# Optimization experiments

Hardware: AMD Instinct MI355X
Metric: run time of the kernel (lower is better)

## Reference

```python
import jax, jax.numpy as jnp
import numpy as np

N = 25000   # nodes
E = 100000  # edges
FN = 32     # num_node_features
FE = 16     # num_edge_features
DH = 32     # node_hidden_channels (= edge_hidden_channels)
H = 4       # gat heads
DG = 8      # gat hidden per head (H*DG == DH)
C = 10      # num_classes


def setup_inputs() -> dict:
    key = jax.random.key(0)
    ks = jax.random.split(key, 25)
    f = lambda k, s: (jax.random.normal(k, s, dtype=jnp.float32) * 0.1)
    inp = {
        "x": jax.random.normal(ks[0], (N, FN), dtype=jnp.float32),
        "edge_attr": jax.random.normal(ks[1], (E, FE), dtype=jnp.float32),
        "edge_index": jax.random.randint(ks[2], (2, E), 0, N, dtype=jnp.int32),
        # node / edge encoders
        "We_node": f(ks[3], (FN, DH)), "be_node": f(ks[4], (DH,)),
        "We_edge": f(ks[5], (FE, DH)), "be_edge": f(ks[6], (DH,)),
        # conv1 (NNConv): edge MLP -> [DH*DH], root weight, bias
        "W1_nn": f(ks[7], (DH, DH * DH)), "b1_nn": f(ks[8], (DH * DH,)),
        "root1": f(ks[9], (DH, DH)), "bias1": f(ks[10], (DH,)),
        # GATv2Conv: lin_l, lin_r (with bias), attention vector, output bias
        "Wl": f(ks[11], (DH, H * DG)), "bl": f(ks[12], (H * DG,)),
        "Wr": f(ks[13], (DH, H * DG)), "br": f(ks[14], (H * DG,)),
        "att": f(ks[15], (H, DG)), "bias_gat": f(ks[16], (H * DG,)),
        # conv2 (NNConv): in = H*DG = 32, out = DH = 32
        "W2_nn": f(ks[17], (DH, H * DG * DH)), "b2_nn": f(ks[18], (H * DG * DH,)),
        "root2": f(ks[19], (H * DG, DH)), "bias2": f(ks[20], (DH,)),
        # final classifier
        "Wlin": f(ks[21], (DH, C)), "blin": f(ks[22], (C,)),
    }
    return inp


def _forward(x, edge_attr, edge_index, We_node, be_node, We_edge, be_edge,
             W1_nn, b1_nn, root1, bias1, Wl, bl, Wr, br, att, bias_gat,
             W2_nn, b2_nn, root2, bias2, Wlin, blin):
    src, dst = edge_index[0], edge_index[1]  # message flows src -> dst
    h = x @ We_node + be_node                # [N, DH]
    ea = edge_attr @ We_edge + be_edge       # [E, DH]

    # ---- NNConv 1: per-edge weight matrices + scatter-add, root + bias ----
    W1 = (ea @ W1_nn + b1_nn).reshape(E, DH, DH)       # [E, DH, DH]
    msg = jnp.einsum('ei,eio->eo', h[src], W1)          # [E, DH]
    agg = jax.ops.segment_sum(msg, dst, num_segments=N)
    h = jax.nn.relu(agg + h @ root1 + bias1)

    # ---- GATv2Conv (adds self loops, like PyG default) ----
    loops = jnp.arange(N, dtype=src.dtype)
    si = jnp.concatenate([src, loops])
    di = jnp.concatenate([dst, loops])
    xl = (h @ Wl + bl).reshape(N, H, DG)
    xr = (h @ Wr + br).reshape(N, H, DG)
    e = jax.nn.leaky_relu(xl[si] + xr[di], negative_slope=0.2)  # [E2, H, DG]
    logits = jnp.einsum('ehd,hd->eh', e, att)                   # [E2, H]
    m = jax.lax.stop_gradient(jax.ops.segment_max(logits, di, num_segments=N))
    m = jnp.where(jnp.isfinite(m), m, 0.0)
    a = jnp.exp(logits - m[di])
    denom = jax.ops.segment_sum(a, di, num_segments=N)
    alpha = a / (denom[di] + 1e-16)                             # segment softmax over dst
    out = jax.ops.segment_sum(xl[si] * alpha[:, :, None], di, num_segments=N)
    h = jax.nn.relu(out.reshape(N, H * DG) + bias_gat)

    # ---- NNConv 2 ----
    W2 = (ea @ W2_nn + b2_nn).reshape(E, H * DG, DH)
    msg2 = jnp.einsum('ei,eio->eo', h[src], W2)
    agg2 = jax.ops.segment_sum(msg2, dst, num_segments=N)
    h = jax.nn.relu(agg2 + h @ root2 + bias2)

    return h @ Wlin + blin


def reference(x, edge_attr, edge_index, We_node, be_node, We_edge, be_edge,
              W1_nn, b1_nn, root1, bias1, Wl, bl, Wr, br, att, bias_gat,
              W2_nn, b2_nn, root2, bias2, Wlin, blin):
    return _forward(x, edge_attr, edge_index, We_node, be_node, We_edge, be_edge,
                    W1_nn, b1_nn, root1, bias1, Wl, bl, Wr, br, att, bias_gat,
                    W2_nn, b2_nn, root2, bias2, Wlin, blin)
```

## Files before the change

### kernel.cpp

```cpp
#include <hip/hip_runtime.h>
#include <hip/hip_bf16.h>
#include <math.h>

#define NN 25000
#define NE 100000
#define NTILES (NE / 16)
#define NBN 98
#define NBE 391
#define NBP 264
#define NBC 391

typedef __attribute__((ext_vector_type(8))) short short8;
typedef __attribute__((ext_vector_type(4))) float f32x4;

static __device__ __forceinline__ short8 pack_bf8(const float* p) {
  union { short8 s; unsigned int u[4]; } r;
#pragma unroll
  for (int q = 0; q < 4; q++)
    asm("v_cvt_pk_bf16_f32 %0, %1, %2" : "=v"(r.u[q]) : "v"(p[2 * q]), "v"(p[2 * q + 1]));
  return r.s;
}

__global__ void __launch_bounds__(256) k_zero(int* __restrict__ deg) {
  int n = blockIdx.x * 256 + threadIdx.x;
  if (n < NN) deg[n] = 0;
}

__global__ void __launch_bounds__(256) k_prep(
    const float* __restrict__ x, const float* __restrict__ eattr,
    const int* __restrict__ ei,
    const float* __restrict__ We_node, const float* __restrict__ be_node,
    const float* __restrict__ We_edge, const float* __restrict__ be_edge,
    const float* __restrict__ root1, const float* __restrict__ bias1,
    const float* __restrict__ W1, const float* __restrict__ b1,
    const float* __restrict__ W2, const float* __restrict__ b2,
    float* __restrict__ h0, float* __restrict__ r1pre, float* __restrict__ ea,
    __hip_bfloat16* __restrict__ Bswz1, __hip_bfloat16* __restrict__ Bswz2,
    int* __restrict__ deg) {
  int b = blockIdx.x;
  int tid = threadIdx.x;
  if (b < NBN) {
    int n = b * 256 + tid;
    if (n >= NN) return;
    float xv[32], hv[32], rv[32];
#pragma unroll
    for (int i = 0; i < 8; i++) *(float4*)(xv + 4 * i) = *(const float4*)(x + n * 32 + 4 * i);
#pragma unroll
    for (int j = 0; j < 32; j++) hv[j] = be_node[j];
#pragma unroll
    for (int i = 0; i < 32; i++) {
      float xi = xv[i];
#pragma unroll
      for (int j = 0; j < 32; j++) hv[j] += xi * We_node[i * 32 + j];
    }
#pragma unroll
    for (int i = 0; i < 8; i++) *(float4*)(h0 + n * 32 + 4 * i) = *(float4*)(hv + 4 * i);
#pragma unroll
    for (int j = 0; j < 32; j++) rv[j] = bias1[j];
#pragma unroll
    for (int i = 0; i < 32; i++) {
      float hi = hv[i];
#pragma unroll
      for (int j = 0; j < 32; j++) rv[j] += hi * root1[i * 32 + j];
    }
#pragma unroll
    for (int i = 0; i < 8; i++) *(float4*)(r1pre + n * 32 + 4 * i) = *(float4*)(rv + 4 * i);
  } else if (b < NBN + NBE) {
    int e = (b - NBN) * 256 + tid;
    if (e >= NE) return;
    float av[16], ov[32];
#pragma unroll
    for (int i = 0; i < 4; i++) *(float4*)(av + 4 * i) = *(const float4*)(eattr + e * 16 + 4 * i);
#pragma unroll
    for (int j = 0; j < 32; j++) ov[j] = be_edge[j];
#pragma unroll
    for (int k = 0; k < 16; k++) {
      float ak = av[k];
#pragma unroll
      for (int j = 0; j < 32; j++) ov[j] += ak * We_edge[k * 32 + j];
    }
#pragma unroll
    for (int i = 0; i < 8; i++) *(float4*)(ea + e * 32 + 4 * i) = *(float4*)(ov + 4 * i);
  } else if (b < NBN + NBE + NBP) {
    int idx = (b - NBN - NBE) * 256 + tid;
    if (idx >= 2 * 33792) return;
    int sel = idx >= 33792;
    int r = idx - sel * 33792;
    int j = r & 7;
    int l = (r >> 3) & 63;
    int nt = (r >> 9) & 1;
    int t = r >> 10;
    int i = 8 * (l >> 4) + j;
    int o = nt * 16 + (l & 15);
    const float* W = sel ? W2 : W1;
    const float* bb = sel ? b2 : b1;
    float v = (t < 32) ? W[t * 1024 + i * 32 + o] : bb[i * 32 + o];
    (sel ? Bswz2 : Bswz1)[r] = __float2bfloat16(v);
  } else {
    int e = (b - NBN - NBE - NBP) * 256 + tid;
    if (e < NE) atomicAdd(&deg[ei[NE + e]], 1);
  }
}

__global__ void __launch_bounds__(256) k_scan1(const int* __restrict__ deg,
                                               int* __restrict__ bsum) {
  __shared__ int s[256];
  int tid = threadIdx.x;
  int n = blockIdx.x * 256 + tid;
  s[tid] = (n < NN) ? deg[n] : 0;
  __syncthreads();
  for (int d = 128; d > 0; d >>= 1) {
    if (tid < d) s[tid] += s[tid + d];
    __syncthreads();
  }
  if (tid == 0) bsum[blockIdx.x] = s[0];
}

__global__ void __launch_bounds__(256) k_scan3(const int* __restrict__ deg,
                                               const int* __restrict__ bsum,
                                               int* __restrict__ off,
                                               int* __restrict__ cursor) {
  __shared__ int sb[128];
  __shared__ int s[256];
  int tid = threadIdx.x;
  if (tid < 128) sb[tid] = (tid < NBN) ? bsum[tid] : 0;
  int n = blockIdx.x * 256 + tid;
  int v = (n < NN) ? deg[n] : 0;
  s[tid] = v;
  __syncthreads();
  for (int d = 1; d < 128; d <<= 1) {
    int t = 0;
    if (tid < 128 && tid >= d) t = sb[tid - d];
    __syncthreads();
    if (tid < 128) sb[tid] += t;
    __syncthreads();
  }
  for (int d = 1; d < 256; d <<= 1) {
    int t = (tid >= d) ? s[tid - d] : 0;
    __syncthreads();
    s[tid] += t;
    __syncthreads();
  }
  int base = (blockIdx.x > 0) ? sb[blockIdx.x - 1] : 0;
  int excl = s[tid] - v + base;
  if (n < NN) { off[n] = excl; cursor[n] = excl; }
}

__global__ void k_csr_fill(const int* __restrict__ ei, int* __restrict__ cursor,
                           int* __restrict__ slot, int* __restrict__ perm) {
  int e = blockIdx.x * blockDim.x + threadIdx.x;
  if (e >= NE) return;
  int d = ei[NE + e];
  int p = atomicAdd(&cursor[d], 1);
  slot[p] = e;
  perm[e] = p;
}

__global__ void __launch_bounds__(256) k_nnconv_mfma(
    const float* __restrict__ hin, const float* __restrict__ ea,
    const __hip_bfloat16* __restrict__ Bswz, const int* __restrict__ ei,
    const int* __restrict__ perm, float* __restrict__ msgbuf) {
  extern __shared__ short8 bsh[];
  int tid = threadIdx.x;
  {
    uint4* s4 = (uint4*)bsh;
    const uint4* g4 = (const uint4*)Bswz;
#pragma unroll
    for (int it = 0; it < 16; it++) s4[tid + 256 * it] = g4[tid + 256 * it];
  }
  __syncthreads();

  int wid = tid >> 6;
  int lane = tid & 63;
  int lrow = lane & 15;
  int lk8 = (lane >> 4) * 8;

  for (int tile = blockIdx.x * 4 + wid; tile < NTILES; tile += gridDim.x * 4) {
    int e0 = tile * 16;
    int e = e0 + lrow;
    int src = ei[e];
    float hf[8];
    *(float4*)(hf)     = *(const float4*)(hin + src * 32 + lk8);
    *(float4*)(hf + 4) = *(const float4*)(hin + src * 32 + lk8 + 4);
    float eav[32];
#pragma unroll
    for (int c = 0; c < 8; c++)
      *(float4*)(eav + 4 * c) = *(const float4*)(ea + e * 32 + 4 * c);
    short8 af_bias = pack_bf8(hf);

    f32x4 a00 = {0.f, 0.f, 0.f, 0.f}, a01 = a00, a10 = a00, a11 = a00;
#pragma unroll
    for (int t = 0; t < 32; t++) {
      float et = eav[t];
      float pr[8];
#pragma unroll
      for (int j = 0; j < 8; j++) pr[j] = et * hf[j];
      short8 af = pack_bf8(pr);
      short8 b0 = bsh[(t * 2 + 0) * 64 + lane];
      short8 b1 = bsh[(t * 2 + 1) * 64 + lane];
      if (t & 1) {
        a01 = __builtin_amdgcn_mfma_f32_16x16x32_bf16(af, b0, a01, 0, 0, 0);
        a11 = __builtin_amdgcn_mfma_f32_16x16x32_bf16(af, b1, a11, 0, 0, 0);
      } else {
        a00 = __builtin_amdgcn_mfma_f32_16x16x32_bf16(af, b0, a00, 0, 0, 0);
        a10 = __builtin_amdgcn_mfma_f32_16x16x32_bf16(af, b1, a10, 0, 0, 0);
      }
    }
    {
      const short8* gb = (const short8*)Bswz;
      short8 b0 = gb[(32 * 2 + 0) * 64 + lane];
      short8 b1 = gb[(32 * 2 + 1) * 64 + lane];
      a00 = __builtin_amdgcn_mfma_f32_16x16x32_bf16(af_bias, b0, a00, 0, 0, 0);
      a10 = __builtin_amdgcn_mfma_f32_16x16x32_bf16(af_bias, b1, a10, 0, 0, 0);
    }
    f32x4 c0 = a00 + a01;
    f32x4 c1 = a10 + a11;
    int r0 = (lane >> 4) * 4;
#pragma unroll
    for (int r = 0; r < 4; r++) {
      int p = perm[e0 + r0 + r];
      float* mp = msgbuf + p * 32 + lrow;
      mp[0]  = c0[r];
      mp[16] = c1[r];
    }
  }
}

__global__ void __launch_bounds__(256) k_node1(
    const float* __restrict__ r1pre, const float* __restrict__ msgbuf,
    const int* __restrict__ off, const int* __restrict__ deg,
    const float* __restrict__ Wl, const float* __restrict__ bl,
    const float* __restrict__ Wr, const float* __restrict__ br,
    float* __restrict__ xl, float* __restrict__ xr) {
  int t = blockIdx.x * blockDim.x + threadIdx.x;
  if (t >= 2 * NN) return;
  int n = t >> 1, half = t & 1;
  int c0 = half * 16;
  float hv[16];
  const float* rp = r1pre + n * 32 + c0;
#pragma unroll
  for (int i = 0; i < 4; i++) *(float4*)(hv + 4 * i) = *(const float4*)(rp + 4 * i);
  int o0 = off[n], o1 = o0 + deg[n];
  for (int idx = o0; idx < o1; idx++) {
    const float* mp = msgbuf + idx * 32 + c0;
#pragma unroll
    for (int i = 0; i < 4; i++) {
      float4 mv = *(const float4*)(mp + 4 * i);
      hv[4 * i + 0] += mv.x; hv[4 * i + 1] += mv.y;
      hv[4 * i + 2] += mv.z; hv[4 * i + 3] += mv.w;
    }
  }
#pragma unroll
  for (int j = 0; j < 16; j++) hv[j] = fmaxf(hv[j], 0.f);
  float a0[16], a1[16];
#pragma unroll
  for (int j = 0; j < 16; j++) {
    float o = __shfl_xor(hv[j], 1);
    a0[j] = half ? o : hv[j];
    a1[j] = half ? hv[j] : o;
  }
  const float* W = half ? Wr : Wl;
  const float* bb = half ? br : bl;
  float ov[32];
#pragma unroll
  for (int j = 0; j < 32; j++) ov[j] = bb[j];
#pragma unroll
  for (int i = 0; i < 16; i++) {
    float u = a0[i], v = a1[i];
#pragma unroll
    for (int j = 0; j < 32; j++)
      ov[j] += u * W[i * 32 + j] + v * W[(16 + i) * 32 + j];
  }
  float* dst = (half ? xr : xl) + n * 32;
#pragma unroll
  for (int i = 0; i < 8; i++) *(float4*)(dst + 4 * i) = *(float4*)(ov + 4 * i);
}

__global__ void __launch_bounds__(256) k_gat_node(
    const int* __restrict__ ei, const int* __restrict__ slot,
    const float* __restrict__ xl, const float* __restrict__ xr,
    const int* __restrict__ off, const int* __restrict__ deg,
    const float* __restrict__ att, const float* __restrict__ bias_gat,
    float* __restrict__ h2) {
  int t = blockIdx.x * blockDim.x + threadIdx.x;
  if (t >= 4 * NN) return;
  int n = t >> 2, hh = t & 3;
  const float* xrp = xr + n * 32 + hh * 8;
  const float* xsp = xl + n * 32 + hh * 8;
  const float* atp = att + hh * 8;
  float xrv[8], attv[8], xself[8];
  *(float4*)(xrv)      = *(const float4*)(xrp);
  *(float4*)(xrv + 4)  = *(const float4*)(xrp + 4);
  *(float4*)(attv)     = *(const float4*)(atp);
  *(float4*)(attv + 4) = *(const float4*)(atp + 4);
  *(float4*)(xself)    = *(const float4*)(xsp);
  *(float4*)(xself + 4)= *(const float4*)(xsp + 4);
  float slg = 0.f;
#pragma unroll
  for (int dg = 0; dg < 8; dg++) {
    float v = xself[dg] + xrv[dg];
    v = (v > 0.f) ? v : 0.2f * v;
    slg += v * attv[dg];
  }
  float w0 = __expf(slg);
  float den = w0;
  float accv[8];
#pragma unroll
  for (int dg = 0; dg < 8; dg++) accv[dg] = w0 * xself[dg];
  int o0 = off[n], o1 = o0 + deg[n];
  for (int idx = o0; idx < o1; idx++) {
    int s = ei[slot[idx]];
    const float* xp = xl + s * 32 + hh * 8;
    float xv[8];
    *(float4*)(xv)     = *(const float4*)(xp);
    *(float4*)(xv + 4) = *(const float4*)(xp + 4);
    float lg = 0.f;
#pragma unroll
    for (int dg = 0; dg < 8; dg++) {
      float v = xv[dg] + xrv[dg];
      v = (v > 0.f) ? v : 0.2f * v;
      lg += v * attv[dg];
    }
    float w = __expf(lg);
    den += w;
#pragma unroll
    for (int dg = 0; dg < 8; dg++) accv[dg] += w * xv[dg];
  }
  float sc = 1.f / (den + 1e-16f);
  float hv[8];
#pragma unroll
  for (int dg = 0; dg < 8; dg++)
    hv[dg] = fmaxf(accv[dg] * sc + bias_gat[hh * 8 + dg], 0.f);
  float* op = h2 + n * 32 + hh * 8;
  *(float4*)(op)     = *(float4*)(hv);
  *(float4*)(op + 4) = *(float4*)(hv + 4);
}

__global__ void __launch_bounds__(256) k_node2(
    const float* __restrict__ h2, const float* __restrict__ msgbuf,
    const int* __restrict__ off, const int* __restrict__ deg,
    const float* __restrict__ root2, const float* __restrict__ bias2,
    const float* __restrict__ Wlin, const float* __restrict__ blin,
    float* __restrict__ out) {
  int t = blockIdx.x * blockDim.x + threadIdx.x;
  if (t >= 2 * NN) return;
  int n = t >> 1, half = t & 1;
  int c0 = half * 16;
  float h2v[32];
#pragma unroll
  for (int i = 0; i < 8; i++) *(float4*)(h2v + 4 * i) = *(const float4*)(h2 + n * 32 + 4 * i);
  float rv[16];
#pragma unroll
  for (int j = 0; j < 16; j++) rv[j] = bias2[c0 + j];
#pragma unroll
  for (int i = 0; i < 32; i++) {
    float hi = h2v[i];
#pragma unroll
    for (int j = 0; j < 16; j++) rv[j] += hi * root2[i * 32 + c0 + j];
  }
  int o0 = off[n], o1 = o0 + deg[n];
  for (int idx = o0; idx < o1; idx++) {
    const float* mp = msgbuf + idx * 32 + c0;
#pragma unroll
    for (int i = 0; i < 4; i++) {
      float4 mv = *(const float4*)(mp + 4 * i);
      rv[4 * i + 0] += mv.x; rv[4 * i + 1] += mv.y;
      rv[4 * i + 2] += mv.z; rv[4 * i + 3] += mv.w;
    }
  }
#pragma unroll
  for (int j = 0; j < 16; j++) rv[j] = fmaxf(rv[j], 0.f);
  float ov[10];
#pragma unroll
  for (int c = 0; c < 10; c++) ov[c] = 0.f;
#pragma unroll
  for (int j = 0; j < 16; j++) {
    float hj = rv[j];
#pragma unroll
    for (int c = 0; c < 10; c++) ov[c] += hj * Wlin[(c0 + j) * 10 + c];
  }
#pragma unroll
  for (int c = 0; c < 10; c++) ov[c] += __shfl_xor(ov[c], 1);
  if (half == 0) {
#pragma unroll
    for (int c = 0; c < 5; c++) out[n * 10 + c] = ov[c] + blin[c];
  } else {
#pragma unroll
    for (int c = 5; c < 10; c++) out[n * 10 + c] = ov[c] + blin[c];
  }
}

extern "C" void kernel_launch(void* const* d_in, const int* in_sizes, int n_in,
                              void* d_out, int out_size, void* d_ws, size_t ws_size,
                              hipStream_t stream) {
  const float* x         = (const float*)d_in[0];
  const float* edge_attr = (const float*)d_in[1];
  const int*   ei        = (const int*)d_in[2];
  const float* We_node   = (const float*)d_in[3];
  const float* be_node   = (const float*)d_in[4];
  const float* We_edge   = (const float*)d_in[5];
  const float* be_edge   = (const float*)d_in[6];
  const float* W1_nn     = (const float*)d_in[7];
  const float* b1_nn     = (const float*)d_in[8];
  const float* root1     = (const float*)d_in[9];
  const float* bias1     = (const float*)d_in[10];
  const float* Wl        = (const float*)d_in[11];
  const float* bl        = (const float*)d_in[12];
  const float* Wr        = (const float*)d_in[13];
  const float* br        = (const float*)d_in[14];
  const float* att       = (const float*)d_in[15];
  const float* bias_gat  = (const float*)d_in[16];
  const float* W2_nn     = (const float*)d_in[17];
  const float* b2_nn     = (const float*)d_in[18];
  const float* root2     = (const float*)d_in[19];
  const float* bias2     = (const float*)d_in[20];
  const float* Wlin      = (const float*)d_in[21];
  const float* blin      = (const float*)d_in[22];
  float* out = (float*)d_out;

  float* ws = (float*)d_ws;
  float* h0h2  = ws;
  float* ea    = h0h2 + NN * 32;
  float* r1pre = ea + NE * 32;
  float* xl    = r1pre + NN * 32;
  float* xr    = xl + NN * 32;
  float* msgbuf = xr + NN * 32;
  float* fend  = msgbuf + NE * 32;
  __hip_bfloat16* Bswz1 = (__hip_bfloat16*)fend;
  __hip_bfloat16* Bswz2 = (__hip_bfloat16*)(fend + 17000);
  int* deg    = (int*)(fend + 34000);
  int* off    = deg + NN;
  int* cursor = off + NN;
  int* bsum   = cursor + NN;
  int* slot   = bsum + 128;
  int* perm   = slot + NE;

  const int B = 256;
  k_zero<<<NBN, B, 0, stream>>>(deg);
  k_prep<<<NBN + NBE + NBP + NBC, B, 0, stream>>>(
      x, edge_attr, ei, We_node, be_node, We_edge, be_edge, root1, bias1,
      W1_nn, b1_nn, W2_nn, b2_nn, h0h2, r1pre, ea, Bswz1, Bswz2, deg);
  k_scan1<<<NBN, B, 0, stream>>>(deg, bsum);
  k_scan3<<<NBN, B, 0, stream>>>(deg, bsum, off, cursor);
  k_csr_fill<<<(NE + B - 1) / B, B, 0, stream>>>(ei, cursor, slot, perm);
  k_nnconv_mfma<<<512, B, 65536, stream>>>(h0h2, ea, Bswz1, ei, perm, msgbuf);
  k_node1<<<(2 * NN + B - 1) / B, B, 0, stream>>>(r1pre, msgbuf, off, deg, Wl, bl, Wr, br, xl, xr);
  k_gat_node<<<(4 * NN + B - 1) / B, B, 0, stream>>>(ei, slot, xl, xr, off, deg, att, bias_gat, h0h2);
  k_nnconv_mfma<<<512, B, 65536, stream>>>(h0h2, ea, Bswz2, ei, perm, msgbuf);
  k_node2<<<(2 * NN + B - 1) / B, B, 0, stream>>>(h0h2, msgbuf, off, deg, root2, bias2, Wlin, blin, out);
}
```

Before: 124.5 us.

## Store edge messages in bf16, precompute CSR sources, split GAT heads across more threads

The per-edge message buffer is now written in bf16 instead of fp32, which halves the scatter-write and gather-read traffic in the NNConv aggregation kernels. The node aggregation loops are unrolled by two to keep more loads in flight. The CSR fill now also writes each sorted edge's source index, removing the double indirection ei[slot[idx]] in the GAT kernel. The GAT kernel uses 8 threads per node, each handling 4 channels and combining half-head logits with a shuffle. The cost is lower message precision and one extra index array written during CSR construction.

Result: faster. 117.9 us (-5.3%).

```diff
diff --git a/kernel.cpp b/kernel.cpp
--- a/kernel.cpp
+++ b/kernel.cpp
@@ -19,6 +19,17 @@
   for (int q = 0; q < 4; q++)
     asm("v_cvt_pk_bf16_f32 %0, %1, %2" : "=v"(r.u[q]) : "v"(p[2 * q]), "v"(p[2 * q + 1]));
   return r.s;
+}
+
+static __device__ __forceinline__ void bfadd8(float* hv, uint4 A) {
+  hv[0] += __uint_as_float(A.x << 16);
+  hv[1] += __uint_as_float(A.x & 0xffff0000u);
+  hv[2] += __uint_as_float(A.y << 16);
+  hv[3] += __uint_as_float(A.y & 0xffff0000u);
+  hv[4] += __uint_as_float(A.z << 16);
+  hv[5] += __uint_as_float(A.z & 0xffff0000u);
+  hv[6] += __uint_as_float(A.w << 16);
+  hv[7] += __uint_as_float(A.w & 0xffff0000u);
 }
 
 __global__ void __launch_bounds__(256) k_zero(int* __restrict__ deg) {
@@ -147,19 +158,21 @@
 }
 
 __global__ void k_csr_fill(const int* __restrict__ ei, int* __restrict__ cursor,
-                           int* __restrict__ slot, int* __restrict__ perm) {
+                           int* __restrict__ slot, int* __restrict__ perm,
+                           int* __restrict__ srcs) {
   int e = blockIdx.x * blockDim.x + threadIdx.x;
   if (e >= NE) return;
   int d = ei[NE + e];
   int p = atomicAdd(&cursor[d], 1);
   slot[p] = e;
   perm[e] = p;
+  srcs[p] = ei[e];
 }
 
 __global__ void __launch_bounds__(256) k_nnconv_mfma(
     const float* __restrict__ hin, const float* __restrict__ ea,
     const __hip_bfloat16* __restrict__ Bswz, const int* __restrict__ ei,
-    const int* __restrict__ perm, float* __restrict__ msgbuf) {
+    const int* __restrict__ perm, __hip_bfloat16* __restrict__ msgbuf) {
   extern __shared__ short8 bsh[];
   int tid = threadIdx.x;
   {
@@ -219,15 +232,15 @@
 #pragma unroll
     for (int r = 0; r < 4; r++) {
       int p = perm[e0 + r0 + r];
-      float* mp = msgbuf + p * 32 + lrow;
-      mp[0]  = c0[r];
-      mp[16] = c1[r];
+      __hip_bfloat16* mp = msgbuf + p * 32 + lrow;
+      mp[0]  = __float2bfloat16(c0[r]);
+      mp[16] = __float2bfloat16(c1[r]);
     }
   }
 }
 
 __global__ void __launch_bounds__(256) k_node1(
-    const float* __restrict__ r1pre, const float* __restrict__ msgbuf,
+    const float* __restrict__ r1pre, const __hip_bfloat16* __restrict__ msgbuf,
     const int* __restrict__ off, const int* __restrict__ deg,
     const float* __restrict__ Wl, const float* __restrict__ bl,
     const float* __restrict__ Wr, const float* __restrict__ br,
@@ -241,14 +254,18 @@
 #pragma unroll
   for (int i = 0; i < 4; i++) *(float4*)(hv + 4 * i) = *(const float4*)(rp + 4 * i);
   int o0 = off[n], o1 = o0 + deg[n];
-  for (int idx = o0; idx < o1; idx++) {
-    const float* mp = msgbuf + idx * 32 + c0;
-#pragma unroll
-    for (int i = 0; i < 4; i++) {
-      float4 mv = *(const float4*)(mp + 4 * i);
-      hv[4 * i + 0] += mv.x; hv[4 * i + 1] += mv.y;
-      hv[4 * i + 2] += mv.z; hv[4 * i + 3] += mv.w;
-    }
+  int idx = o0;
+  for (; idx + 1 < o1; idx += 2) {
+    const uint4* mp = (const uint4*)(msgbuf + idx * 32 + c0);
+    const uint4* mq = (const uint4*)(msgbuf + (idx + 1) * 32 + c0);
+    uint4 A0 = mp[0], B0 = mp[1], A1 = mq[0], B1 = mq[1];
+    bfadd8(hv, A0); bfadd8(hv + 8, B0);
+    bfadd8(hv, A1); bfadd8(hv + 8, B1);
+  }
+  if (idx < o1) {
+    const uint4* mp = (const uint4*)(msgbuf + idx * 32 + c0);
+    uint4 A0 = mp[0], B0 = mp[1];
+    bfadd8(hv, A0); bfadd8(hv + 8, B0);
   }
 #pragma unroll
   for (int j = 0; j < 16; j++) hv[j] = fmaxf(hv[j], 0.f);
@@ -277,67 +294,83 @@
 }
 
 __global__ void __launch_bounds__(256) k_gat_node(
-    const int* __restrict__ ei, const int* __restrict__ slot,
+    const int* __restrict__ srcs,
     const float* __restrict__ xl, const float* __restrict__ xr,
     const int* __restrict__ off, const int* __restrict__ deg,
     const float* __restrict__ att, const float* __restrict__ bias_gat,
     float* __restrict__ h2) {
   int t = blockIdx.x * blockDim.x + threadIdx.x;
-  if (t >= 4 * NN) return;
-  int n = t >> 2, hh = t & 3;
-  const float* xrp = xr + n * 32 + hh * 8;
-  const float* xsp = xl + n * 32 + hh * 8;
-  const float* atp = att + hh * 8;
-  float xrv[8], attv[8], xself[8];
-  *(float4*)(xrv)      = *(const float4*)(xrp);
-  *(float4*)(xrv + 4)  = *(const float4*)(xrp + 4);
-  *(float4*)(attv)     = *(const float4*)(atp);
-  *(float4*)(attv + 4) = *(const float4*)(atp + 4);
-  *(float4*)(xself)    = *(const float4*)(xsp);
-  *(float4*)(xself + 4)= *(const float4*)(xsp + 4);
-  float slg = 0.f;
-#pragma unroll
-  for (int dg = 0; dg < 8; dg++) {
+  if (t >= 8 * NN) return;
+  int n = t >> 3, sub = t & 7;
+  int co = sub * 4;
+  float xrv[4], attv[4], xself[4];
+  *(float4*)(xrv)   = *(const float4*)(xr + n * 32 + co);
+  *(float4*)(attv)  = *(const float4*)(att + co);
+  *(float4*)(xself) = *(const float4*)(xl + n * 32 + co);
+  float slgp = 0.f;
+#pragma unroll
+  for (int dg = 0; dg < 4; dg++) {
     float v = xself[dg] + xrv[dg];
     v = (v > 0.f) ? v : 0.2f * v;
-    slg += v * attv[dg];
-  }
+    slgp += v * attv[dg];
+  }
+  float slg = slgp + __shfl_xor(slgp, 1);
   float w0 = __expf(slg);
   float den = w0;
-  float accv[8];
-#pragma unroll
-  for (int dg = 0; dg < 8; dg++) accv[dg] = w0 * xself[dg];
+  float accv[4];
+#pragma unroll
+  for (int dg = 0; dg < 4; dg++) accv[dg] = w0 * xself[dg];
   int o0 = off[n], o1 = o0 + deg[n];
-  for (int idx = o0; idx < o1; idx++) {
-    int s = ei[slot[idx]];
-    const float* xp = xl + s * 32 + hh * 8;
-    float xv[8];
-    *(float4*)(xv)     = *(const float4*)(xp);
-    *(float4*)(xv + 4) = *(const float4*)(xp + 4);
-    float lg = 0.f;
-#pragma unroll
-    for (int dg = 0; dg < 8; dg++) {
-      float v = xv[dg] + xrv[dg];
-      v = (v > 0.f) ? v : 0.2f * v;
-      lg += v * attv[dg];
-    }
-    float w = __expf(lg);
-    den += w;
-#pragma unroll
-    for (int dg = 0; dg < 8; dg++) accv[dg] += w * xv[dg];
+  int idx = o0;
+  for (; idx + 1 < o1; idx += 2) {
+    int s0 = srcs[idx], s1 = srcs[idx + 1];
+    float xa[4], xb[4];
+    *(float4*)(xa) = *(const float4*)(xl + s0 * 32 + co);
+    *(float4*)(xb) = *(const float4*)(xl + s1 * 32 + co);
+    float lga = 0.f, lgb = 0.f;
+#pragma unroll
+    for (int dg = 0; dg < 4; dg++) {
+      float va = xa[dg] + xrv[dg];
+      va = (va > 0.f) ? va : 0.2f * va;
+      lga += va * attv[dg];
+      float vb = xb[dg] + xrv[dg];
+      vb = (vb > 0.f) ? vb : 0.2f * vb;
+      lgb += vb * attv[dg];
+    }
+    float la = lga + __shfl_xor(lga, 1);
+    float lb = lgb + __shfl_xor(lgb, 1);
+    float wa = __expf(la), wb = __expf(lb);
+    den += wa + wb;
+#pragma unroll
+    for (int dg = 0; dg < 4; dg++) accv[dg] += wa * xa[dg] + wb * xb[dg];
+  }
+  if (idx < o1) {
+    int s0 = srcs[idx];
+    float xa[4];
+    *(float4*)(xa) = *(const float4*)(xl + s0 * 32 + co);
+    float lga = 0.f;
+#pragma unroll
+    for (int dg = 0; dg < 4; dg++) {
+      float va = xa[dg] + xrv[dg];
+      va = (va > 0.f) ? va : 0.2f * va;
+      lga += va * attv[dg];
+    }
+    float la = lga + __shfl_xor(lga, 1);
+    float wa = __expf(la);
+    den += wa;
+#pragma unroll
+    for (int dg = 0; dg < 4; dg++) accv[dg] += wa * xa[dg];
   }
   float sc = 1.f / (den + 1e-16f);
-  float hv[8];
-#pragma unroll
-  for (int dg = 0; dg < 8; dg++)
-    hv[dg] = fmaxf(accv[dg] * sc + bias_gat[hh * 8 + dg], 0.f);
-  float* op = h2 + n * 32 + hh * 8;
-  *(float4*)(op)     = *(float4*)(hv);
-  *(float4*)(op + 4) = *(float4*)(hv + 4);
+  float hv[4];
+#pragma unroll
+  for (int dg = 0; dg < 4; dg++)
+    hv[dg] = fmaxf(accv[dg] * sc + bias_gat[co + dg], 0.f);
+  *(float4*)(h2 + n * 32 + co) = *(float4*)(hv);
 }
 
 __global__ void __launch_bounds__(256) k_node2(
-    const float* __restrict__ h2, const float* __restrict__ msgbuf,
+    const float* __restrict__ h2, const __hip_bfloat16* __restrict__ msgbuf,
     const int* __restrict__ off, const int* __restrict__ deg,
     const float* __restrict__ root2, const float* __restrict__ bias2,
     const float* __restrict__ Wlin, const float* __restrict__ blin,
@@ -359,14 +392,18 @@
     for (int j = 0; j < 16; j++) rv[j] += hi * root2[i * 32 + c0 + j];
   }
   int o0 = off[n], o1 = o0 + deg[n];
-  for (int idx = o0; idx < o1; idx++) {
-    const float* mp = msgbuf + idx * 32 + c0;
-#pragma unroll
-    for (int i = 0; i < 4; i++) {
-      float4 mv = *(const float4*)(mp + 4 * i);
-      rv[4 * i + 0] += mv.x; rv[4 * i + 1] += mv.y;
-      rv[4 * i + 2] += mv.z; rv[4 * i + 3] += mv.w;
-    }
+  int idx = o0;
+  for (; idx + 1 < o1; idx += 2) {
+    const uint4* mp = (const uint4*)(msgbuf + idx * 32 + c0);
+    const uint4* mq = (const uint4*)(msgbuf + (idx + 1) * 32 + c0);
+    uint4 A0 = mp[0], B0 = mp[1], A1 = mq[0], B1 = mq[1];
+    bfadd8(rv, A0); bfadd8(rv + 8, B0);
+    bfadd8(rv, A1); bfadd8(rv + 8, B1);
+  }
+  if (idx < o1) {
+    const uint4* mp = (const uint4*)(msgbuf + idx * 32 + c0);
+    uint4 A0 = mp[0], B0 = mp[1];
+    bfadd8(rv, A0); bfadd8(rv + 8, B0);
   }
 #pragma unroll
   for (int j = 0; j < 16; j++) rv[j] = fmaxf(rv[j], 0.f);
@@ -424,8 +461,9 @@
   float* r1pre = ea + NE * 32;
   float* xl    = r1pre + NN * 32;
   float* xr    = xl + NN * 32;
-  float* msgbuf = xr + NN * 32;
-  float* fend  = msgbuf + NE * 32;
+  float* mslab = xr + NN * 32;
+  __hip_bfloat16* msgbuf = (__hip_bfloat16*)mslab;
+  float* fend  = mslab + NE * 32;
   __hip_bfloat16* Bswz1 = (__hip_bfloat16*)fend;
   __hip_bfloat16* Bswz2 = (__hip_bfloat16*)(fend + 17000);
   int* deg    = (int*)(fend + 34000);
@@ -434,6 +472,7 @@
   int* bsum   = cursor + NN;
   int* slot   = bsum + 128;
   int* perm   = slot + NE;
+  int* srcs   = perm + NE;
 
   const int B = 256;
   k_zero<<<NBN, B, 0, stream>>>(deg);
@@ -442,10 +481,10 @@
       W1_nn, b1_nn, W2_nn, b2_nn, h0h2, r1pre, ea, Bswz1, Bswz2, deg);
   k_scan1<<<NBN, B, 0, stream>>>(deg, bsum);
   k_scan3<<<NBN, B, 0, stream>>>(deg, bsum, off, cursor);
-  k_csr_fill<<<(NE + B - 1) / B, B, 0, stream>>>(ei, cursor, slot, perm);
+  k_csr_fill<<<(NE + B - 1) / B, B, 0, stream>>>(ei, cursor, slot, perm, srcs);
   k_nnconv_mfma<<<512, B, 65536, stream>>>(h0h2, ea, Bswz1, ei, perm, msgbuf);
   k_node1<<<(2 * NN + B - 1) / B, B, 0, stream>>>(r1pre, msgbuf, off, deg, Wl, bl, Wr, br, xl, xr);
-  k_gat_node<<<(4 * NN + B - 1) / B, B, 0, stream>>>(ei, slot, xl, xr, off, deg, att, bias_gat, h0h2);
+  k_gat_node<<<(8 * NN + B - 1) / B, B, 0, stream>>>(srcs, xl, xr, off, deg, att, bias_gat, h0h2);
   k_nnconv_mfma<<<512, B, 65536, stream>>>(h0h2, ea, Bswz2, ei, perm, msgbuf);
   k_node2<<<(2 * NN + B - 1) / B, B, 0, stream>>>(h0h2, msgbuf, off, deg, root2, bias2, Wlin, blin, out);
 }
```
